# Performance work log

Measured on AMD Instinct MI355X. Metric: run time of the kernel, lower is better.

## Reference

```python
import jax, jax.numpy as jnp
import numpy as np

N_NODES = 100000
N_EDGES = 1600000
D_FEAT = 256
HIDDEN = 256
OUT = 128


def _glorot(key, shape):
    fan_in, fan_out = shape[1], shape[0]
    lim = float(np.sqrt(6.0 / (fan_in + fan_out)))
    return jax.random.uniform(key, shape, jnp.float32, -lim, lim)


def setup_inputs() -> dict:
    key = jax.random.key(0)
    ks = jax.random.split(key, 12)
    x = jax.random.normal(ks[0], (N_NODES, D_FEAT), jnp.float32)
    edge_index = jax.random.randint(ks[1], (2, N_EDGES), 0, N_NODES, jnp.int64)
    return {
        "x": x,
        "edge_index": edge_index,
        # SAGEConv1: lin_l (neighbors, has bias), lin_r (root, no bias)
        "W1l": _glorot(ks[2], (HIDDEN, D_FEAT)),
        "b1l": jnp.zeros((HIDDEN,), jnp.float32),
        "W1r": _glorot(ks[3], (HIDDEN, D_FEAT)),
        # SAGEConv2
        "W2l": _glorot(ks[4], (OUT, HIDDEN)),
        "b2l": jnp.zeros((OUT,), jnp.float32),
        "W2r": _glorot(ks[5], (OUT, HIDDEN)),
        # EdgeDecoder
        "Wd1": _glorot(ks[6], (OUT, 2 * OUT)),
        "bd1": jnp.zeros((OUT,), jnp.float32),
        "Wd2": _glorot(ks[7], (1, OUT)),
        "bd2": jnp.zeros((1,), jnp.float32),
    }


def _sage_conv(x, src, dst, Wl, bl, Wr):
    # mean-aggregate source features into destination nodes (PyG SAGEConv, aggr='mean')
    msg_sum = jax.ops.segment_sum(x[src], dst, num_segments=N_NODES)  # [N, d]
    cnt = jax.ops.segment_sum(jnp.ones((src.shape[0],), x.dtype), dst, num_segments=N_NODES)
    mean = msg_sum / jnp.maximum(cnt, 1.0)[:, None]
    return mean @ Wl.T + bl + x @ Wr.T


def reference(x, edge_index, W1l, b1l, W1r, W2l, b2l, W2r, Wd1, bd1, Wd2, bd2):
    src, dst = edge_index[0], edge_index[1]
    # NodeEncoder
    h = jax.nn.relu(_sage_conv(x, src, dst, W1l, b1l, W1r))
    z = _sage_conv(h, src, dst, W2l, b2l, W2r)  # [N, OUT]
    # EdgeDecoder: gather per-edge endpoint embeddings, concat, MLP
    zc = jnp.concatenate([z[src], z[dst]], axis=-1)  # [E, 2*OUT]
    hd = jax.nn.relu(zc @ Wd1.T + bd1)
    out = hd @ Wd2.T + bd2  # [E, 1]
    return out.reshape(-1)
```

## Files before the change

kernel.cpp:

```cpp
#include <hip/hip_runtime.h>
#include <stdint.h>

static constexpr int NN = 100000;
static constexpr int NE = 1600000;
static constexpr int NB_SCAN = (NN + 255) / 256;
static constexpr int NB_CVTX = NN * 256 / 4 / 256;
static constexpr int NB_HIST = NE / 256;
static constexpr int NB_CVTW = 897;

typedef __bf16 bf16;
typedef __bf16 bf16x4 __attribute__((ext_vector_type(4)));
typedef __bf16 bf16x8 __attribute__((ext_vector_type(8)));
typedef float floatx4 __attribute__((ext_vector_type(4)));

__device__ __forceinline__ void async16(const void* g, void* l) {
  __builtin_amdgcn_global_load_lds(
      (const __attribute__((address_space(1))) void*)g,
      (__attribute__((address_space(3))) void*)l, 16, 0, 0);
}

__device__ __forceinline__ uint32_t pk4_fp8(float a, float b, float c, float d) {
  uint32_t v = 0;
  v = (uint32_t)__builtin_amdgcn_cvt_pk_fp8_f32(a, b, (int)v, false);
  v = (uint32_t)__builtin_amdgcn_cvt_pk_fp8_f32(c, d, (int)v, true);
  return v;
}

__device__ __forceinline__ void acc_fp8x8(float* a, uint2 v) {
  a[0] += __builtin_amdgcn_cvt_f32_fp8(v.x, 0);
  a[1] += __builtin_amdgcn_cvt_f32_fp8(v.x, 1);
  a[2] += __builtin_amdgcn_cvt_f32_fp8(v.x, 2);
  a[3] += __builtin_amdgcn_cvt_f32_fp8(v.x, 3);
  a[4] += __builtin_amdgcn_cvt_f32_fp8(v.y, 0);
  a[5] += __builtin_amdgcn_cvt_f32_fp8(v.y, 1);
  a[6] += __builtin_amdgcn_cvt_f32_fp8(v.y, 2);
  a[7] += __builtin_amdgcn_cvt_f32_fp8(v.y, 3);
}

__device__ __forceinline__ int clampN(int c) {
  return ((unsigned)c < (unsigned)NN) ? c : 0;
}

__global__ void k_cvtx_hist(const float* __restrict__ x, bf16* __restrict__ xb,
                            uint32_t* __restrict__ xq,
                            const int* __restrict__ dst, int* __restrict__ cnt8,
                            uint16_t* __restrict__ rank) {
  int b = blockIdx.x;
  int m = b % 5;
  if (m < 4) {
    int cb = (b / 5) * 4 + m;
    int t = cb * 256 + threadIdx.x;
    const float4 v = ((const float4*)x)[t];
    bf16x4 o;
    o.x = (bf16)v.x; o.y = (bf16)v.y; o.z = (bf16)v.z; o.w = (bf16)v.w;
    ((bf16x4*)xb)[t] = o;
    xq[t] = pk4_fp8(v.x, v.y, v.z, v.w);
  } else {
    int hb = b / 5;
    int e = hb * 256 + threadIdx.x;
    uint32_t xcd;
    asm("s_getreg_b32 %0, hwreg(HW_REG_XCC_ID)" : "=s"(xcd));
    xcd &= 7u;
    int d = dst[e];
    int old = __hip_atomic_fetch_add(&cnt8[(size_t)xcd * NN + d], 1,
                                     __ATOMIC_RELAXED, __HIP_MEMORY_SCOPE_WORKGROUP);
    rank[e] = (uint16_t)((xcd << 12) | ((uint32_t)old & 0xFFFu));
  }
}

__global__ void k_cvtw_scanpart(
    const float* __restrict__ W1l, const float* __restrict__ W1r,
    const float* __restrict__ W2l, const float* __restrict__ W2r,
    const float* __restrict__ Wd1, const float* __restrict__ bd1,
    bf16* __restrict__ B1, bf16* __restrict__ B2,
    bf16* __restrict__ Bd, float* __restrict__ biasPQ,
    const int* __restrict__ cnt8, int* __restrict__ part, int N) {
  int b = blockIdx.x;
  if (b < NB_CVTW) {
    int g = b * 256 + threadIdx.x;
    if (g < 131072) {
      int o = g >> 9, k = g & 511;
      float v = (k < 256) ? W1l[o * 256 + k] : W1r[o * 256 + k - 256];
      B1[g] = (bf16)v;
    } else if (g < 131072 + 65536) {
      int t = g - 131072;
      int o = t >> 8, k = t & 255;
      float v = (o < 128) ? W2l[o * 256 + k] : W2r[(o - 128) * 256 + k];
      B2[t] = (bf16)v;
    } else if (g < 131072 + 65536 + 32768) {
      int t = g - 196608;
      int o = t >> 7, k = t & 127;
      float v = (o < 128) ? Wd1[o * 256 + k] : Wd1[(o - 128) * 256 + 128 + k];
      Bd[t] = (bf16)v;
    } else if (g < 131072 + 65536 + 32768 + 256) {
      int t = g - 229376;
      biasPQ[t] = (t < 128) ? bd1[t] : 0.0f;
    }
  } else {
    __shared__ int sh[256];
    int bb = b - NB_CVTW;
    int t = threadIdx.x;
    int i = bb * 256 + t;
    int tot = 0;
    if (i < N) {
#pragma unroll
      for (int xx = 0; xx < 8; ++xx) tot += cnt8[(size_t)xx * NN + i];
    }
    sh[t] = tot;
    __syncthreads();
    for (int off = 128; off > 0; off >>= 1) {
      if (t < off) sh[t] += sh[t + off];
      __syncthreads();
    }
    if (t == 0) part[bb] = sh[0];
  }
}

__global__ __launch_bounds__(512) void k_scan_mid(int* __restrict__ part, int NB) {
  __shared__ int sh[512];
  int t = threadIdx.x;
  int v = (t < NB) ? part[t] : 0;
  sh[t] = v;
  __syncthreads();
  for (int off = 1; off < 512; off <<= 1) {
    int u = (t >= off) ? sh[t - off] : 0;
    __syncthreads();
    sh[t] += u;
    __syncthreads();
  }
  if (t < NB) part[t] = sh[t] - v;
}

__global__ void k_scan_fin(int* __restrict__ cnt8, const int* __restrict__ part,
                           int* __restrict__ rowptr, int N, int E) {
  __shared__ int sh[256];
  int t = threadIdx.x;
  int i = blockIdx.x * 256 + t;
  int c[8];
  int v = 0;
  if (i < N) {
#pragma unroll
    for (int xx = 0; xx < 8; ++xx) { c[xx] = cnt8[(size_t)xx * NN + i]; v += c[xx]; }
  } else {
#pragma unroll
    for (int xx = 0; xx < 8; ++xx) c[xx] = 0;
  }
  sh[t] = v;
  __syncthreads();
  for (int off = 1; off < 256; off <<= 1) {
    int u = (t >= off) ? sh[t - off] : 0;
    __syncthreads();
    sh[t] += u;
    __syncthreads();
  }
  if (i < N) {
    int base = part[blockIdx.x] + sh[t] - v;
    rowptr[i] = base;
#pragma unroll
    for (int xx = 0; xx < 8; ++xx) { cnt8[(size_t)xx * NN + i] = base; base += c[xx]; }
  }
  if (i == 0) rowptr[N] = E;
}

__global__ void k_fill(const int* __restrict__ src, const int* __restrict__ dst,
                       const int* __restrict__ rptr8,
                       const uint16_t* __restrict__ rank,
                       int* __restrict__ csr, int E) {
  int e = blockIdx.x * 256 + threadIdx.x;
  if (e < E) {
    int d = dst[e];
    uint32_t rv = rank[e];
    int pos = rptr8[(size_t)(rv >> 12) * NN + d] + (int)(rv & 0xFFFu);
    if ((unsigned)pos >= (unsigned)E) pos = 0;
    csr[pos] = src[e];
  }
}

__global__ void k_agg(const uint8_t* __restrict__ xq, const int* __restrict__ rowptr,
                      const int* __restrict__ csr, bf16* __restrict__ mean) {
  int wave = threadIdx.x >> 6, lane = threadIdx.x & 63;
  int n = blockIdx.x * 4 + wave;
  int s = rowptr[n], e = rowptr[n + 1];
  int half = lane >> 5, l32 = lane & 31;
  float a[8] = {};
  const uint8_t* base = xq + l32 * 8;
  int i = s + half;
  for (; i + 6 < e; i += 8) {
    int c0 = clampN(csr[i]), c1 = clampN(csr[i + 2]);
    int c2 = clampN(csr[i + 4]), c3 = clampN(csr[i + 6]);
    uint2 v0 = *(const uint2*)(base + (size_t)c0 * 256);
    uint2 v1 = *(const uint2*)(base + (size_t)c1 * 256);
    uint2 v2 = *(const uint2*)(base + (size_t)c2 * 256);
    uint2 v3 = *(const uint2*)(base + (size_t)c3 * 256);
    acc_fp8x8(a, v0); acc_fp8x8(a, v1); acc_fp8x8(a, v2); acc_fp8x8(a, v3);
  }
  for (; i < e; i += 2) {
    uint2 v = *(const uint2*)(base + (size_t)clampN(csr[i]) * 256);
    acc_fp8x8(a, v);
  }
  int deg = e - s;
  float sc = 1.0f / (float)(deg > 0 ? deg : 1);
  bf16x8 o;
#pragma unroll
  for (int j = 0; j < 8; ++j) {
    float t = a[j] + __shfl_xor(a[j], 32);
    o[j] = (bf16)(t * sc);
  }
  if (half == 0)
    *(bf16x8*)(mean + (size_t)n * 256 + l32 * 8) = o;
}

__global__ void k_agg2z(const uint8_t* __restrict__ hq, const bf16* __restrict__ hr,
                        const int* __restrict__ rowptr, const int* __restrict__ csr,
                        const float* __restrict__ b2l, bf16* __restrict__ zf) {
  int wave = threadIdx.x >> 6, lane = threadIdx.x & 63;
  int n = blockIdx.x * 4 + wave;
  int s = rowptr[n], e = rowptr[n + 1];
  int sub = lane >> 4, l16 = lane & 15;
  float a[8] = {};
  const uint8_t* base = hq + l16 * 8;
  int i = s + sub;
  for (; i + 4 < e; i += 8) {
    int c0 = clampN(csr[i]), c1 = clampN(csr[i + 4]);
    uint2 v0 = *(const uint2*)(base + (size_t)c0 * 128);
    uint2 v1 = *(const uint2*)(base + (size_t)c1 * 128);
    acc_fp8x8(a, v0); acc_fp8x8(a, v1);
  }
  for (; i < e; i += 4) {
    uint2 v = *(const uint2*)(base + (size_t)clampN(csr[i]) * 128);
    acc_fp8x8(a, v);
  }
  int deg = e - s;
  float sc = 1.0f / (float)(deg > 0 ? deg : 1);
  bf16x8 hv = *(const bf16x8*)(hr + (size_t)n * 128 + l16 * 8);
  const float4* b4 = (const float4*)(b2l + l16 * 8);
  float4 ba = b4[0], bb = b4[1];
  float bl[8] = {ba.x, ba.y, ba.z, ba.w, bb.x, bb.y, bb.z, bb.w};
  bf16x8 o;
#pragma unroll
  for (int j = 0; j < 8; ++j) {
    float t = a[j];
    t += __shfl_xor(t, 16);
    t += __shfl_xor(t, 32);
    o[j] = (bf16)(t * sc + (float)hv[j] + bl[j]);
  }
  if (sub == 0)
    *(bf16x8*)(zf + (size_t)n * 128 + l16 * 8) = o;
}

__global__ __launch_bounds__(256) void k_fused12(
    const bf16* __restrict__ A1, const bf16* __restrict__ A2,
    const bf16* __restrict__ B1, const float* __restrict__ b1l,
    const bf16* __restrict__ B2, uint8_t* __restrict__ hq,
    bf16* __restrict__ hr, int Nrows) {
  __shared__ bf16 Hs[64 * 256];
  __shared__ bf16 As[64 * 64];
  __shared__ bf16 Bs[256 * 64];
  const int tid = threadIdx.x, wave = tid >> 6, lane = tid & 63;
  const int quad = lane >> 4, l16 = lane & 15;
  const int rowBase = blockIdx.x * 64;
  const int wr = (wave >> 1) * 32;
  const int wc = (wave & 1) * 128;
  floatx4 acc[2][8] = {};

  for (int kc = 0; kc < 8; ++kc) {
    const bf16* Asrc = (kc < 4) ? A1 : A2;
    const int kb = (kc & 3) * 64;
    {
      int u = wave * 128 + lane;
      int row = u >> 3, seg = u & 7;
      int sg = seg ^ (row & 7);
      int node = rowBase + row;
      if (node >= Nrows) node = Nrows - 1;
      async16(Asrc + (size_t)node * 256 + kb + sg * 8, &As[(wave * 128) * 8]);
      u += 64;
      row = u >> 3; seg = u & 7;
      sg = seg ^ (row & 7);
      node = rowBase + row;
      if (node >= Nrows) node = Nrows - 1;
      async16(Asrc + (size_t)node * 256 + kb + sg * 8, &As[(wave * 128 + 64) * 8]);
    }
    for (int i = 0; i < 8; ++i) {
      int u = wave * 512 + i * 64 + lane;
      int row = u >> 3, seg = u & 7;
      int sg = seg ^ (row & 7);
      async16(B1 + (size_t)row * 512 + kc * 64 + sg * 8, &Bs[(wave * 512 + i * 64) * 8]);
    }
    __syncthreads();
    for (int ks = 0; ks < 2; ++ks) {
      bf16x8 af[2], bq[8];
      const int sw = (ks * 4 + quad) ^ (l16 & 7);
      for (int mt = 0; mt < 2; ++mt)
        af[mt] = *(const bf16x8*)&As[(wr + mt * 16 + l16) * 64 + sw * 8];
      for (int nt = 0; nt < 8; ++nt)
        bq[nt] = *(const bf16x8*)&Bs[(wc + nt * 16 + l16) * 64 + sw * 8];
      for (int mt = 0; mt < 2; ++mt)
        for (int nt = 0; nt < 8; ++nt)
          acc[mt][nt] = __builtin_amdgcn_mfma_f32_16x16x32_bf16(af[mt], bq[nt], acc[mt][nt], 0, 0, 0);
    }
    __syncthreads();
  }

  {
    float bv1[8];
    for (int nt = 0; nt < 8; ++nt) bv1[nt] = b1l[wc + nt * 16 + l16];
    for (int mt = 0; mt < 2; ++mt)
      for (int nt = 0; nt < 8; ++nt) {
        int col = wc + nt * 16 + l16;
        int c = col >> 3;
        for (int r = 0; r < 4; ++r) {
          int row = wr + mt * 16 + quad * 4 + r;
          float v = fmaxf(acc[mt][nt][r] + bv1[nt], 0.0f);
          Hs[row * 256 + (c ^ (row & 7)) * 8 + (col & 7)] = (bf16)v;
          acc[mt][nt][r] = 0.0f;
        }
      }
  }
  __syncthreads();

  for (int kc = 0; kc < 4; ++kc) {
    for (int i = 0; i < 8; ++i) {
      int u = wave * 512 + i * 64 + lane;
      int row = u >> 3, seg = u & 7;
      int sg = seg ^ (row & 7);
      async16(B2 + (size_t)row * 256 + kc * 64 + sg * 8, &Bs[(wave * 512 + i * 64) * 8]);
    }
    __syncthreads();
    for (int ks = 0; ks < 2; ++ks) {
      bf16x8 af[2], bq[8];
      const int swb = (ks * 4 + quad) ^ (l16 & 7);
      const int ck = kc * 8 + ks * 4 + quad;
      for (int mt = 0; mt < 2; ++mt) {
        int row = wr + mt * 16 + l16;
        af[mt] = *(const bf16x8*)&Hs[row * 256 + (ck ^ (row & 7)) * 8];
      }
      for (int nt = 0; nt < 8; ++nt)
        bq[nt] = *(const bf16x8*)&Bs[(wc + nt * 16 + l16) * 64 + swb * 8];
      for (int mt = 0; mt < 2; ++mt)
        for (int nt = 0; nt < 8; ++nt)
          acc[mt][nt] = __builtin_amdgcn_mfma_f32_16x16x32_bf16(af[mt], bq[nt], acc[mt][nt], 0, 0, 0);
    }
    __syncthreads();
  }

  for (int mt = 0; mt < 2; ++mt)
    for (int nt = 0; nt < 8; ++nt) {
      int oc = wc + nt * 16 + l16;
      for (int r = 0; r < 4; ++r) {
        int grow = rowBase + wr + mt * 16 + quad * 4 + r;
        if (grow < Nrows) {
          float v = acc[mt][nt][r];
          if (oc < 128) {
            uint32_t pk = (uint32_t)__builtin_amdgcn_cvt_pk_fp8_f32(v, v, 0, false);
            hq[(size_t)grow * 128 + oc] = (uint8_t)pk;
          } else {
            hr[(size_t)grow * 128 + oc - 128] = (bf16)v;
          }
        }
      }
    }
}

template <int KDIM, int EPI>
__global__ __launch_bounds__(256) void k_gemm(
    const bf16* __restrict__ A, const bf16* __restrict__ B,
    const float* __restrict__ bias, void* __restrict__ out1,
    void* __restrict__ out2, int Nrows) {
  __shared__ bf16 As[128 * 64];
  __shared__ bf16 Bs[128 * 64];
  const int tid = threadIdx.x, wave = tid >> 6, lane = tid & 63;
  const int quad = lane >> 4, l16 = lane & 15;
  const int rowBase = blockIdx.y * 128;
  const int colBase = blockIdx.x * 128;
  const int wr = (wave >> 1) * 64;
  const int wc = (wave & 1) * 64;
  floatx4 acc[4][4] = {};

  for (int kc = 0; kc < KDIM / 64; ++kc) {
    for (int i = 0; i < 4; ++i) {
      int u = wave * 256 + i * 64 + lane;
      int row = u >> 3, seg = u & 7;
      int sg = seg ^ (row & 7);
      int node = rowBase + row;
      if (node >= Nrows) node = Nrows - 1;
      async16(A + (size_t)node * KDIM + kc * 64 + sg * 8, &As[(wave * 256 + i * 64) * 8]);
    }
    for (int i = 0; i < 4; ++i) {
      int u = wave * 256 + i * 64 + lane;
      int row = u >> 3, seg = u & 7;
      int sg = seg ^ (row & 7);
      async16(B + (size_t)(colBase + row) * KDIM + kc * 64 + sg * 8,
              &Bs[(wave * 256 + i * 64) * 8]);
    }
    __syncthreads();
    for (int ks = 0; ks < 2; ++ks) {
      bf16x8 af[4], bq[4];
      const int sw = (ks * 4 + quad) ^ (l16 & 7);
      for (int mt = 0; mt < 4; ++mt)
        af[mt] = *(const bf16x8*)&As[(wr + mt * 16 + l16) * 64 + sw * 8];
      for (int nt = 0; nt < 4; ++nt)
        bq[nt] = *(const bf16x8*)&Bs[(wc + nt * 16 + l16) * 64 + sw * 8];
      for (int mt = 0; mt < 4; ++mt)
        for (int nt = 0; nt < 4; ++nt)
          acc[mt][nt] = __builtin_amdgcn_mfma_f32_16x16x32_bf16(af[mt], bq[nt], acc[mt][nt], 0, 0, 0);
    }
    __syncthreads();
  }
  float bv[4];
  for (int nt = 0; nt < 4; ++nt)
    bv[nt] = (EPI == 2) ? bias[colBase + wc + nt * 16 + l16] : 0.0f;
  const bool lowHalf = (colBase == 0);
  for (int mt = 0; mt < 4; ++mt)
    for (int nt = 0; nt < 4; ++nt) {
      int gcol = colBase + wc + nt * 16 + l16;
      for (int r = 0; r < 4; ++r) {
        int grow = rowBase + wr + mt * 16 + quad * 4 + r;
        if (grow < Nrows) {
          float v = acc[mt][nt][r] + bv[nt];
          if (lowHalf) {
            if (EPI == 1) {
              uint32_t pk = (uint32_t)__builtin_amdgcn_cvt_pk_fp8_f32(v, v, 0, false);
              ((uint8_t*)out1)[(size_t)grow * 128 + gcol] = (uint8_t)pk;
            } else {
              ((bf16*)out1)[(size_t)grow * 128 + gcol] = (bf16)v;
            }
          } else {
            ((bf16*)out2)[(size_t)grow * 128 + gcol - 128] = (bf16)v;
          }
        }
      }
    }
}

__global__ __launch_bounds__(256) void k_edge(
    const bf16* __restrict__ P, const bf16* __restrict__ Q,
    const int* __restrict__ rowptr, const int* __restrict__ csr,
    const float* __restrict__ wd2, const float* __restrict__ bd2,
    float* __restrict__ outCSR) {
  int wave = threadIdx.x >> 6, lane = threadIdx.x & 63;
  int n = blockIdx.x * 4 + wave;
  int s = rowptr[n], e = rowptr[n + 1];
  int sub = lane >> 4, l16 = lane & 15;
  bf16x8 qv = *(const bf16x8*)(Q + (size_t)n * 128 + l16 * 8);
  float qf[8];
#pragma unroll
  for (int j = 0; j < 8; ++j) qf[j] = (float)qv[j];
  const float4* w4 = (const float4*)(wd2 + l16 * 8);
  float4 wa = w4[0], wb = w4[1];
  float w[8] = {wa.x, wa.y, wa.z, wa.w, wb.x, wb.y, wb.z, wb.w};
  const float bout = bd2[0];
  int i = s + sub;
  for (; i + 4 < e; i += 8) {
    int c0 = clampN(csr[i]), c1 = clampN(csr[i + 4]);
    bf16x8 p0 = *(const bf16x8*)(P + (size_t)c0 * 128 + l16 * 8);
    bf16x8 p1 = *(const bf16x8*)(P + (size_t)c1 * 128 + l16 * 8);
    float a0 = 0.f, a1 = 0.f;
#pragma unroll
    for (int j = 0; j < 8; ++j) {
      a0 += fmaxf((float)p0[j] + qf[j], 0.f) * w[j];
      a1 += fmaxf((float)p1[j] + qf[j], 0.f) * w[j];
    }
    a0 += __shfl_xor(a0, 1); a1 += __shfl_xor(a1, 1);
    a0 += __shfl_xor(a0, 2); a1 += __shfl_xor(a1, 2);
    a0 += __shfl_xor(a0, 4); a1 += __shfl_xor(a1, 4);
    a0 += __shfl_xor(a0, 8); a1 += __shfl_xor(a1, 8);
    if (l16 == 0) { outCSR[i] = a0 + bout; outCSR[i + 4] = a1 + bout; }
  }
  for (; i < e; i += 4) {
    int c = clampN(csr[i]);
    bf16x8 p = *(const bf16x8*)(P + (size_t)c * 128 + l16 * 8);
    float a = 0.f;
#pragma unroll
    for (int j = 0; j < 8; ++j)
      a += fmaxf((float)p[j] + qf[j], 0.f) * w[j];
    a += __shfl_xor(a, 1);
    a += __shfl_xor(a, 2);
    a += __shfl_xor(a, 4);
    a += __shfl_xor(a, 8);
    if (l16 == 0) outCSR[i] = a + bout;
  }
}

__global__ void k_perm(const int* __restrict__ dst, const uint16_t* __restrict__ rank,
                       const int* __restrict__ rptr8, const float* __restrict__ outCSR,
                       float* __restrict__ out, int E) {
  int e = blockIdx.x * 256 + threadIdx.x;
  if (e < E) {
    int d = dst[e];
    uint32_t rv = rank[e];
    int pos = rptr8[(size_t)(rv >> 12) * NN + d] + (int)(rv & 0xFFFu);
    if ((unsigned)pos >= (unsigned)E) pos = 0;
    out[e] = outCSR[pos];
  }
}

extern "C" void kernel_launch(void* const* d_in, const int* in_sizes, int n_in,
                              void* d_out, int out_size, void* d_ws, size_t ws_size,
                              hipStream_t stream) {
  const float* x   = (const float*)d_in[0];
  const int*   ei  = (const int*)d_in[1];
  const float* W1l = (const float*)d_in[2];
  const float* b1l = (const float*)d_in[3];
  const float* W1r = (const float*)d_in[4];
  const float* W2l = (const float*)d_in[5];
  const float* b2l = (const float*)d_in[6];
  const float* W2r = (const float*)d_in[7];
  const float* Wd1 = (const float*)d_in[8];
  const float* bd1 = (const float*)d_in[9];
  const float* Wd2 = (const float*)d_in[10];
  const float* bd2 = (const float*)d_in[11];
  float* out = (float*)d_out;

  const int N = NN, E = NE;
  const int* srcv = ei;
  const int* dstv = ei + E;

  char* w = (char*)d_ws;
  size_t off = 0;
  auto take = [&](size_t bytes) {
    size_t o = off;
    off = (off + bytes + 255) & ~(size_t)255;
    return o;
  };
  int*      cnt8   = (int*)(w + take((size_t)8 * N * 4));
  int*      rowptr = (int*)(w + take((size_t)(N + 1) * 4));
  int*      part   = (int*)(w + take((size_t)NB_SCAN * 4));
  uint16_t* rank   = (uint16_t*)(w + take((size_t)E * 2));
  int*      csr    = (int*)(w + take((size_t)E * 4));
  bf16*     xb     = (bf16*)(w + take((size_t)N * 256 * 2));
  uint8_t*  xq     = (uint8_t*)(w + take((size_t)N * 256));
  bf16*     mean   = (bf16*)(w + take((size_t)N * 256 * 2));
  bf16*     h      = (bf16*)(w + take((size_t)N * 256 * 2));
  bf16*     zf     = (bf16*)(w + take((size_t)N * 128 * 2));
  bf16*     B1     = (bf16*)(w + take((size_t)131072 * 2));
  bf16*     B2     = (bf16*)(w + take((size_t)65536 * 2));
  bf16*     Bd     = (bf16*)(w + take((size_t)32768 * 2));
  float*    biasPQ = (float*)(w + take((size_t)256 * 4));
  int*     rptr8 = cnt8;
  float*   outCSR = (float*)xb;
  uint8_t* hq = (uint8_t*)h;
  bf16*    hr = (bf16*)(hq + (size_t)N * 128);
  bf16*    P  = mean;
  bf16*    Q  = mean + (size_t)N * 128;
  (void)ws_size; (void)n_in; (void)in_sizes; (void)out_size;

  hipMemsetAsync(cnt8, 0, (size_t)8 * N * 4, stream);

  k_cvtx_hist<<<NB_CVTX + NB_HIST, 256, 0, stream>>>(x, xb, (uint32_t*)xq, dstv, cnt8, rank);
  k_cvtw_scanpart<<<NB_CVTW + NB_SCAN, 256, 0, stream>>>(
      W1l, W1r, W2l, W2r, Wd1, bd1, B1, B2, Bd, biasPQ, cnt8, part, N);
  k_scan_mid<<<1, 512, 0, stream>>>(part, NB_SCAN);
  k_scan_fin<<<NB_SCAN, 256, 0, stream>>>(cnt8, part, rowptr, N, E);
  k_fill<<<E / 256, 256, 0, stream>>>(srcv, dstv, rptr8, rank, csr, E);

  k_agg<<<N / 4, 256, 0, stream>>>(xq, rowptr, csr, mean);
  k_fused12<<<(NN + 63) / 64, 256, 0, stream>>>(mean, xb, B1, b1l, B2, hq, hr, N);
  k_agg2z<<<N / 4, 256, 0, stream>>>(hq, hr, rowptr, csr, b2l, zf);
  k_gemm<128, 2><<<dim3(2, 782), 256, 0, stream>>>(zf, Bd, biasPQ, P, Q, N);
  k_edge<<<N / 4, 256, 0, stream>>>(P, Q, rowptr, csr, Wd2, bd2, outCSR);
  k_perm<<<E / 256, 256, 0, stream>>>(dstv, rank, rptr8, outCSR, out, E);
}
```

Measured before the change: 560.4 us.

## Process two 64-row tiles per block in fused layer-1 GEMM to reuse B loads

Each block of the fused two-GEMM kernel now covers 128 rows as two 64-row A tiles sharing the same staged B1 tile. This halves the global-to-LDS traffic for the large 256x512 weight per output row and halves the block count. The second GEMM and epilogue run sequentially per tile through a lambda. The cost is double the accumulator registers (launch bounds set to 2 blocks per SM), more LDS, and fewer blocks to spread across CUs.

```diff
diff --git a/kernel.cpp b/kernel.cpp
--- a/kernel.cpp
+++ b/kernel.cpp
@@ -248,37 +248,37 @@
     *(bf16x8*)(zf + (size_t)n * 128 + l16 * 8) = o;
 }
 
-__global__ __launch_bounds__(256) void k_fused12(
+__global__ __launch_bounds__(256, 2) void k_fused12(
     const bf16* __restrict__ A1, const bf16* __restrict__ A2,
     const bf16* __restrict__ B1, const float* __restrict__ b1l,
     const bf16* __restrict__ B2, uint8_t* __restrict__ hq,
     bf16* __restrict__ hr, int Nrows) {
   __shared__ bf16 Hs[64 * 256];
-  __shared__ bf16 As[64 * 64];
+  __shared__ bf16 As[2][64 * 64];
   __shared__ bf16 Bs[256 * 64];
   const int tid = threadIdx.x, wave = tid >> 6, lane = tid & 63;
   const int quad = lane >> 4, l16 = lane & 15;
-  const int rowBase = blockIdx.x * 64;
+  const int rowBase = blockIdx.x * 128;
   const int wr = (wave >> 1) * 32;
   const int wc = (wave & 1) * 128;
-  floatx4 acc[2][8] = {};
+  floatx4 acc0[2][8] = {};
+  floatx4 acc1[2][8] = {};
 
   for (int kc = 0; kc < 8; ++kc) {
     const bf16* Asrc = (kc < 4) ? A1 : A2;
     const int kb = (kc & 3) * 64;
-    {
-      int u = wave * 128 + lane;
-      int row = u >> 3, seg = u & 7;
-      int sg = seg ^ (row & 7);
-      int node = rowBase + row;
-      if (node >= Nrows) node = Nrows - 1;
-      async16(Asrc + (size_t)node * 256 + kb + sg * 8, &As[(wave * 128) * 8]);
-      u += 64;
-      row = u >> 3; seg = u & 7;
-      sg = seg ^ (row & 7);
-      node = rowBase + row;
-      if (node >= Nrows) node = Nrows - 1;
-      async16(Asrc + (size_t)node * 256 + kb + sg * 8, &As[(wave * 128 + 64) * 8]);
+#pragma unroll
+    for (int t = 0; t < 2; ++t) {
+#pragma unroll
+      for (int i = 0; i < 2; ++i) {
+        int u = wave * 128 + i * 64 + lane;
+        int row = u >> 3, seg = u & 7;
+        int sg = seg ^ (row & 7);
+        int node = rowBase + t * 64 + row;
+        if (node >= Nrows) node = Nrows - 1;
+        async16(Asrc + (size_t)node * 256 + kb + sg * 8,
+                &As[t][(wave * 128 + i * 64) * 8]);
+      }
     }
     for (int i = 0; i < 8; ++i) {
       int u = wave * 512 + i * 64 + lane;
@@ -288,26 +288,44 @@
     }
     __syncthreads();
     for (int ks = 0; ks < 2; ++ks) {
-      bf16x8 af[2], bq[8];
       const int sw = (ks * 4 + quad) ^ (l16 & 7);
-      for (int mt = 0; mt < 2; ++mt)
-        af[mt] = *(const bf16x8*)&As[(wr + mt * 16 + l16) * 64 + sw * 8];
+      bf16x8 bq[8];
+#pragma unroll
       for (int nt = 0; nt < 8; ++nt)
         bq[nt] = *(const bf16x8*)&Bs[(wc + nt * 16 + l16) * 64 + sw * 8];
+      bf16x8 af[2];
+#pragma unroll
       for (int mt = 0; mt < 2; ++mt)
+        af[mt] = *(const bf16x8*)&As[0][(wr + mt * 16 + l16) * 64 + sw * 8];
+#pragma unroll
+      for (int mt = 0; mt < 2; ++mt)
+#pragma unroll
         for (int nt = 0; nt < 8; ++nt)
-          acc[mt][nt] = __builtin_amdgcn_mfma_f32_16x16x32_bf16(af[mt], bq[nt], acc[mt][nt], 0, 0, 0);
-    }
-    __syncthreads();
-  }
-
-  {
-    float bv1[8];
-    for (int nt = 0; nt < 8; ++nt) bv1[nt] = b1l[wc + nt * 16 + l16];
+          acc0[mt][nt] = __builtin_amdgcn_mfma_f32_16x16x32_bf16(af[mt], bq[nt], acc0[mt][nt], 0, 0, 0);
+#pragma unroll
+      for (int mt = 0; mt < 2; ++mt)
+        af[mt] = *(const bf16x8*)&As[1][(wr + mt * 16 + l16) * 64 + sw * 8];
+#pragma unroll
+      for (int mt = 0; mt < 2; ++mt)
+#pragma unroll
+        for (int nt = 0; nt < 8; ++nt)
+          acc1[mt][nt] = __builtin_amdgcn_mfma_f32_16x16x32_bf16(af[mt], bq[nt], acc1[mt][nt], 0, 0, 0);
+    }
+    __syncthreads();
+  }
+
+  float bv1[8];
+#pragma unroll
+  for (int nt = 0; nt < 8; ++nt) bv1[nt] = b1l[wc + nt * 16 + l16];
+
+  auto tile_tail = [&](floatx4 (&acc)[2][8], int t) {
+#pragma unroll
     for (int mt = 0; mt < 2; ++mt)
+#pragma unroll
       for (int nt = 0; nt < 8; ++nt) {
         int col = wc + nt * 16 + l16;
         int c = col >> 3;
+#pragma unroll
         for (int r = 0; r < 4; ++r) {
           int row = wr + mt * 16 + quad * 4 + r;
           float v = fmaxf(acc[mt][nt][r] + bv1[nt], 0.0f);
@@ -315,50 +333,61 @@
           acc[mt][nt][r] = 0.0f;
         }
       }
-  }
-  __syncthreads();
-
-  for (int kc = 0; kc < 4; ++kc) {
-    for (int i = 0; i < 8; ++i) {
-      int u = wave * 512 + i * 64 + lane;
-      int row = u >> 3, seg = u & 7;
-      int sg = seg ^ (row & 7);
-      async16(B2 + (size_t)row * 256 + kc * 64 + sg * 8, &Bs[(wave * 512 + i * 64) * 8]);
-    }
-    __syncthreads();
-    for (int ks = 0; ks < 2; ++ks) {
-      bf16x8 af[2], bq[8];
-      const int swb = (ks * 4 + quad) ^ (l16 & 7);
-      const int ck = kc * 8 + ks * 4 + quad;
-      for (int mt = 0; mt < 2; ++mt) {
-        int row = wr + mt * 16 + l16;
-        af[mt] = *(const bf16x8*)&Hs[row * 256 + (ck ^ (row & 7)) * 8];
+    __syncthreads();
+
+    for (int kc = 0; kc < 4; ++kc) {
+      for (int i = 0; i < 8; ++i) {
+        int u = wave * 512 + i * 64 + lane;
+        int row = u >> 3, seg = u & 7;
+        int sg = seg ^ (row & 7);
+        async16(B2 + (size_t)row * 256 + kc * 64 + sg * 8, &Bs[(wave * 512 + i * 64) * 8]);
       }
-      for (int nt = 0; nt < 8; ++nt)
-        bq[nt] = *(const bf16x8*)&Bs[(wc + nt * 16 + l16) * 64 + swb * 8];
-      for (int mt = 0; mt < 2; ++mt)
+      __syncthreads();
+#pragma unroll
+      for (int ks = 0; ks < 2; ++ks) {
+        const int swb = (ks * 4 + quad) ^ (l16 & 7);
+        const int ck = kc * 8 + ks * 4 + quad;
+        bf16x8 af[2], bq[8];
+#pragma unroll
+        for (int mt = 0; mt < 2; ++mt) {
+          int row = wr + mt * 16 + l16;
+          af[mt] = *(const bf16x8*)&Hs[row * 256 + (ck ^ (row & 7)) * 8];
+        }
+#pragma unroll
         for (int nt = 0; nt < 8; ++nt)
-          acc[mt][nt] = __builtin_amdgcn_mfma_f32_16x16x32_bf16(af[mt], bq[nt], acc[mt][nt], 0, 0, 0);
-    }
-    __syncthreads();
-  }
-
-  for (int mt = 0; mt < 2; ++mt)
-    for (int nt = 0; nt < 8; ++nt) {
-      int oc = wc + nt * 16 + l16;
-      for (int r = 0; r < 4; ++r) {
-        int grow = rowBase + wr + mt * 16 + quad * 4 + r;
-        if (grow < Nrows) {
-          float v = acc[mt][nt][r];
-          if (oc < 128) {
-            uint32_t pk = (uint32_t)__builtin_amdgcn_cvt_pk_fp8_f32(v, v, 0, false);
-            hq[(size_t)grow * 128 + oc] = (uint8_t)pk;
-          } else {
-            hr[(size_t)grow * 128 + oc - 128] = (bf16)v;
+          bq[nt] = *(const bf16x8*)&Bs[(wc + nt * 16 + l16) * 64 + swb * 8];
+#pragma unroll
+        for (int mt = 0; mt < 2; ++mt)
+#pragma unroll
+          for (int nt = 0; nt < 8; ++nt)
+            acc[mt][nt] = __builtin_amdgcn_mfma_f32_16x16x32_bf16(af[mt], bq[nt], acc[mt][nt], 0, 0, 0);
+      }
+      __syncthreads();
+    }
+
+#pragma unroll
+    for (int mt = 0; mt < 2; ++mt)
+#pragma unroll
+      for (int nt = 0; nt < 8; ++nt) {
+        int oc = wc + nt * 16 + l16;
+#pragma unroll
+        for (int r = 0; r < 4; ++r) {
+          int grow = rowBase + t * 64 + wr + mt * 16 + quad * 4 + r;
+          if (grow < Nrows) {
+            float v = acc[mt][nt][r];
+            if (oc < 128) {
+              uint32_t pk = (uint32_t)__builtin_amdgcn_cvt_pk_fp8_f32(v, v, 0, false);
+              hq[(size_t)grow * 128 + oc] = (uint8_t)pk;
+            } else {
+              hr[(size_t)grow * 128 + oc - 128] = (bf16)v;
+            }
           }
         }
       }
-    }
+  };
+
+  tile_tail(acc0, 0);
+  tile_tail(acc1, 1);
 }
 
 template <int KDIM, int EPI>
@@ -554,7 +583,7 @@
   k_fill<<<E / 256, 256, 0, stream>>>(srcv, dstv, rptr8, rank, csr, E);
 
   k_agg<<<N / 4, 256, 0, stream>>>(xq, rowptr, csr, mean);
-  k_fused12<<<(NN + 63) / 64, 256, 0, stream>>>(mean, xb, B1, b1l, B2, hq, hr, N);
+  k_fused12<<<(NN + 127) / 128, 256, 0, stream>>>(mean, xb, B1, b1l, B2, hq, hr, N);
   k_agg2z<<<N / 4, 256, 0, stream>>>(hq, hr, rowptr, csr, b2l, zf);
   k_gemm<128, 2><<<dim3(2, 782), 256, 0, stream>>>(zf, Bd, biasPQ, P, Q, N);
   k_edge<<<N / 4, 256, 0, stream>>>(P, Q, rowptr, csr, Wd2, bd2, outCSR);
```

Result: slower. 590.6 us (+5.4%).
